# Kernel tuning notes

Hardware: AMD Instinct MI355X
Metric: run time of the kernel (lower is better)

## Reference

```python
import jax, jax.numpy as jnp
import numpy as np

N_NODES = 100000
N_EDGES = 1600000
NEG_SLOPE = 0.2  # PyG GATConv default
BN_EPS = 1e-5


def gat_conv(x, src, dst, W, a_src, a_dst, bias):
    # x: [N, F], W: [F, H, C]
    h = jnp.einsum('nf,fhc->nhc', x, W)                 # [N, H, C]
    al_src = jnp.sum(h * a_src, axis=-1)                # [N, H]
    al_dst = jnp.sum(h * a_dst, axis=-1)                # [N, H]
    e = al_src[src] + al_dst[dst]                       # [E, H]
    e = jnp.where(e >= 0, e, NEG_SLOPE * e)             # leaky_relu(0.2)
    # segment softmax over incoming edges of each dst node
    emax = jax.ops.segment_max(e, dst, num_segments=N_NODES)
    ee = jnp.exp(e - emax[dst])
    denom = jax.ops.segment_sum(ee, dst, num_segments=N_NODES)
    alpha = ee / denom[dst]                             # [E, H]
    msg = alpha[:, :, None] * h[src]                    # [E, H, C]
    out = jax.ops.segment_sum(msg, dst, num_segments=N_NODES)  # [N, H, C]
    return out.mean(axis=1) + bias                      # concat=False -> head mean


def batch_norm(x, gamma, beta):
    mu = jnp.mean(x, axis=0)
    var = jnp.var(x, axis=0)  # biased, as in torch BN normalization
    return (x - mu) * jax.lax.rsqrt(var + BN_EPS) * gamma + beta


def setup_inputs() -> dict:
    key = jax.random.key(0)
    ks = jax.random.split(key, 16)
    inp = {
        'x': jax.random.normal(ks[0], (N_NODES, 128), jnp.float32),
        'edge_index': jax.random.randint(ks[1], (2, N_EDGES), 0, N_NODES, jnp.int64)
            if jax.config.jax_enable_x64 else
            jax.random.randint(ks[1], (2, N_EDGES), 0, N_NODES, jnp.int32),
        'edge_attr': jax.random.normal(ks[2], (N_EDGES, 8), jnp.float32),
        'W0': 0.1 * jax.random.normal(ks[3], (128, 4, 32), jnp.float32),
        'a_src0': 0.1 * jax.random.normal(ks[4], (4, 32), jnp.float32),
        'a_dst0': 0.1 * jax.random.normal(ks[5], (4, 32), jnp.float32),
        'b0': jnp.zeros((32,), jnp.float32),
        'g0': jnp.ones((32,), jnp.float32),
        'be0': jnp.zeros((32,), jnp.float32),
        'W1': 0.1 * jax.random.normal(ks[6], (32, 4, 32), jnp.float32),
        'a_src1': 0.1 * jax.random.normal(ks[7], (4, 32), jnp.float32),
        'a_dst1': 0.1 * jax.random.normal(ks[8], (4, 32), jnp.float32),
        'b1': jnp.zeros((32,), jnp.float32),
        'g1': jnp.ones((32,), jnp.float32),
        'be1': jnp.zeros((32,), jnp.float32),
        'W2': 0.1 * jax.random.normal(ks[9], (32, 4, 32), jnp.float32),
        'a_src2': 0.1 * jax.random.normal(ks[10], (4, 32), jnp.float32),
        'a_dst2': 0.1 * jax.random.normal(ks[11], (4, 32), jnp.float32),
        'b2': jnp.zeros((32,), jnp.float32),
    }
    return inp


def reference(x, edge_index, edge_attr, W0, a_src0, a_dst0, b0, g0, be0,
              W1, a_src1, a_dst1, b1, g1, be1, W2, a_src2, a_dst2, b2):
    src, dst = edge_index[0], edge_index[1]
    h = gat_conv(x, src, dst, W0, a_src0, a_dst0, b0)
    h = jax.nn.relu(batch_norm(h, g0, be0))  # dropout = identity (deterministic ref)
    h = gat_conv(h, src, dst, W1, a_src1, a_dst1, b1)
    h = jax.nn.relu(batch_norm(h, g1, be1))
    h = gat_conv(h, src, dst, W2, a_src2, a_dst2, b2)
    return (h, edge_attr)
```

## Files before the change

kernel.cpp:

```cpp
#include <hip/hip_runtime.h>
#include <cstdio>
#include <cstdint>

#define LRELU 0.2f
#define BN_EPS 1e-5f

typedef short bf16x8 __attribute__((ext_vector_type(8)));
typedef float f32x4 __attribute__((ext_vector_type(4)));

__device__ inline unsigned short f2bf(float f) {
  unsigned int u = __float_as_uint(f);
  u += 0x7fffu + ((u >> 16) & 1u);
  return (unsigned short)(u >> 16);
}
__device__ inline float bf2f(unsigned short v) {
  return __uint_as_float(((unsigned int)v) << 16);
}
__device__ inline float bflo(unsigned int u) { return __uint_as_float(u << 16); }
__device__ inline float bfhi(unsigned int u) { return __uint_as_float(u & 0xffff0000u); }


__global__ __launch_bounds__(256) void k_bhist_copy(const int* __restrict__ dst,
                                                    int* __restrict__ bh,
                                                    const float4* __restrict__ ea,
                                                    float4* __restrict__ oea,
                                                    int E) {
  __shared__ int cnt[512];
  for (int b = threadIdx.x; b < 512; b += 256) cnt[b] = 0;
  __syncthreads();
  const int gid = blockIdx.x * blockDim.x + threadIdx.x;
  const int gstride = gridDim.x * blockDim.x;
  for (int i = gid; i < E; i += gstride) atomicAdd(&cnt[dst[i] >> 8], 1);
  const int n4 = E * 2;
  for (int i = gid; i < n4; i += gstride) oea[i] = ea[i];
  __syncthreads();
  for (int b = threadIdx.x; b < 512; b += 256)
    if (cnt[b]) atomicAdd(&bh[b], cnt[b]);
}

__global__ __launch_bounds__(512) void k_exscan(const int* __restrict__ bh,
                                                int* __restrict__ bstart,
                                                int* __restrict__ bcur, int n,
                                                int* __restrict__ offsN) {
  __shared__ int sh[512];
  const int t = threadIdx.x;
  int v = (t < n) ? bh[t] : 0;
  sh[t] = v;
  __syncthreads();
  for (int s = 1; s < 512; s <<= 1) {
    int u = (t >= s) ? sh[t - s] : 0;
    __syncthreads();
    sh[t] += u;
    __syncthreads();
  }
  if (t < n) {
    int ex = sh[t] - v;
    bstart[t] = ex;
    bcur[t] = ex;
  }
  if (t == n - 1) {
    bstart[n] = sh[t];
    *offsN = sh[t];
  }
}

__global__ __launch_bounds__(256) void k_bscatter(const int* __restrict__ src,
                                                  const int* __restrict__ dst,
                                                  int* __restrict__ bcur,
                                                  uint2* __restrict__ bpair, int E) {
  __shared__ int cnt[512];
  const int chunk = (E + gridDim.x - 1) / gridDim.x;
  const int beg = blockIdx.x * chunk;
  const int end = min(E, beg + chunk);
  for (int b = threadIdx.x; b < 512; b += 256) cnt[b] = 0;
  __syncthreads();
  for (int e = beg + threadIdx.x; e < end; e += 256)
    atomicAdd(&cnt[dst[e] >> 8], 1);
  __syncthreads();
  for (int b = threadIdx.x; b < 512; b += 256) {
    int c = cnt[b];
    cnt[b] = (c > 0) ? atomicAdd(&bcur[b], c) : 0;
  }
  __syncthreads();
  for (int e = beg + threadIdx.x; e < end; e += 256) {
    int d = dst[e];
    int pos = atomicAdd(&cnt[d >> 8], 1);
    bpair[pos] = make_uint2((unsigned)src[e], (unsigned)d);
  }
}

__global__ __launch_bounds__(256) void k_bcsr2(const uint2* __restrict__ bpair,
                                               const int* __restrict__ bstart,
                                               int* __restrict__ offs,
                                               int* __restrict__ srcs, int N) {
  __shared__ int sc[256];
  __shared__ int cur[256];
  const int b = blockIdx.x;
  const int lo = b << 8;
  const int t = threadIdx.x;
  const int e0 = bstart[b], e1 = bstart[b + 1];
  sc[t] = 0;
  __syncthreads();
  for (int e = e0 + t; e < e1; e += 256) atomicAdd(&sc[bpair[e].y & 255], 1);
  __syncthreads();
  int v = sc[t];
  for (int s = 1; s < 256; s <<= 1) {
    int u = (t >= s) ? sc[t - s] : 0;
    __syncthreads();
    sc[t] += u;
    __syncthreads();
  }
  const int pos0 = e0 + sc[t] - v;
  cur[t] = pos0;
  if (lo + t < N) offs[lo + t] = pos0;
  __syncthreads();
  for (int e = e0 + t; e < e1; e += 256) {
    uint2 p = bpair[e];
    int pos = atomicAdd(&cur[p.y & 255], 1);
    srcs[pos] = (int)p.x;
  }
}

__global__ void k_castW3(const float* __restrict__ W0, const float* __restrict__ W1,
                         const float* __restrict__ W2,
                         unsigned short* __restrict__ Wt0,
                         unsigned short* __restrict__ Wt1,
                         unsigned short* __restrict__ Wt2) {
  int o = blockIdx.x * 256 + threadIdx.x;
  if (o < 16384) {
    int n = o >> 7, k = o & 127;
    Wt0[o] = f2bf(W0[k * 128 + n]);
  } else if (o < 20480) {
    int p = o - 16384, n = p >> 5, k = p & 31;
    Wt1[p] = f2bf(W1[k * 128 + n]);
  } else if (o < 24576) {
    int p = o - 20480, n = p >> 5, k = p & 31;
    Wt2[p] = f2bf(W2[k * 128 + n]);
  }
}

template <int K, bool BN>
__global__ __launch_bounds__(256) void k_mfma(
    const float* __restrict__ Ain, const unsigned short* __restrict__ Wt,
    const float* __restrict__ asrc, const float* __restrict__ adst,
    const float* __restrict__ stats, const float* __restrict__ g,
    const float* __restrict__ be,
    unsigned short* __restrict__ h, float* __restrict__ als,
    float* __restrict__ ald, int N) {
  __shared__ unsigned short lsh[4][16 * 132];
  __shared__ float sc_s[32], sh_s[32];
  const int wv   = threadIdx.x >> 6;
  const int lane = threadIdx.x & 63;
  const int quad = lane >> 4;
  const int col  = lane & 15;
  const int m0   = blockIdx.x * 64 + wv * 16;
  const int rowc = min(m0 + col, N - 1);

  if constexpr (BN) {
    if (threadIdx.x < 32) {
      float s = 0.f, ss = 0.f;
#pragma unroll
      for (int r = 0; r < 8; r++) {
        s  += stats[r * 64 + threadIdx.x];
        ss += stats[r * 64 + 32 + threadIdx.x];
      }
      const float inv = 1.f / (float)N;
      const float mu = s * inv;
      const float var = ss * inv - mu * mu;
      const float scv = g[threadIdx.x] * rsqrtf(var + BN_EPS);
      sc_s[threadIdx.x] = scv;
      sh_s[threadIdx.x] = be[threadIdx.x] - mu * scv;
    }
    __syncthreads();
  }

  f32x4 acc[8];
#pragma unroll
  for (int t = 0; t < 8; t++) acc[t] = (f32x4){0.f, 0.f, 0.f, 0.f};

#pragma unroll
  for (int ks = 0; ks < K / 32; ks++) {
    const int k0 = ks * 32 + quad * 8;
    const float* ap = Ain + (size_t)rowc * K + k0;
    float4 f0 = *(const float4*)ap;
    float4 f1 = *(const float4*)(ap + 4);
    bf16x8 a;
    if constexpr (BN) {
      f0.x = fmaxf(0.f, fmaf(f0.x, sc_s[k0 + 0], sh_s[k0 + 0]));
      f0.y = fmaxf(0.f, fmaf(f0.y, sc_s[k0 + 1], sh_s[k0 + 1]));
      f0.z = fmaxf(0.f, fmaf(f0.z, sc_s[k0 + 2], sh_s[k0 + 2]));
      f0.w = fmaxf(0.f, fmaf(f0.w, sc_s[k0 + 3], sh_s[k0 + 3]));
      f1.x = fmaxf(0.f, fmaf(f1.x, sc_s[k0 + 4], sh_s[k0 + 4]));
      f1.y = fmaxf(0.f, fmaf(f1.y, sc_s[k0 + 5], sh_s[k0 + 5]));
      f1.z = fmaxf(0.f, fmaf(f1.z, sc_s[k0 + 6], sh_s[k0 + 6]));
      f1.w = fmaxf(0.f, fmaf(f1.w, sc_s[k0 + 7], sh_s[k0 + 7]));
    }
    a[0] = (short)f2bf(f0.x); a[1] = (short)f2bf(f0.y);
    a[2] = (short)f2bf(f0.z); a[3] = (short)f2bf(f0.w);
    a[4] = (short)f2bf(f1.x); a[5] = (short)f2bf(f1.y);
    a[6] = (short)f2bf(f1.z); a[7] = (short)f2bf(f1.w);
#pragma unroll
    for (int t = 0; t < 8; t++) {
      bf16x8 b = *(const bf16x8*)(Wt + (size_t)(t * 16 + col) * K + k0);
      acc[t] = __builtin_amdgcn_mfma_f32_16x16x32_bf16(a, b, acc[t], 0, 0, 0);
    }
  }

#pragma unroll
  for (int t = 0; t < 8; t++) {
#pragma unroll
    for (int j = 0; j < 4; j++)
      lsh[wv][(quad * 4 + j) * 132 + col + 16 * t] = f2bf(acc[t][j]);
  }
  __syncthreads();

  float as8[8], ad8[8];
#pragma unroll
  for (int j = 0; j < 8; j++) {
    as8[j] = asrc[col * 8 + j];
    ad8[j] = adst[col * 8 + j];
  }

#pragma unroll
  for (int i = 0; i < 4; i++) {
    const int row = i * 4 + quad;
    const int hrow = m0 + row;
    const unsigned short* rp = &lsh[wv][row * 132 + col * 8];
    ushort4 lo = *(const ushort4*)rp;
    ushort4 hi = *(const ushort4*)(rp + 4);
    float p = 0.f, q = 0.f, v;
    v = bf2f(lo.x); p += v * as8[0]; q += v * ad8[0];
    v = bf2f(lo.y); p += v * as8[1]; q += v * ad8[1];
    v = bf2f(lo.z); p += v * as8[2]; q += v * ad8[2];
    v = bf2f(lo.w); p += v * as8[3]; q += v * ad8[3];
    v = bf2f(hi.x); p += v * as8[4]; q += v * ad8[4];
    v = bf2f(hi.y); p += v * as8[5]; q += v * ad8[5];
    v = bf2f(hi.z); p += v * as8[6]; q += v * ad8[6];
    v = bf2f(hi.w); p += v * as8[7]; q += v * ad8[7];
    if (hrow < N) {
      ushort4* gp = (ushort4*)(h + (size_t)hrow * 128 + col * 8);
      gp[0] = lo; gp[1] = hi;
    }
    p += __shfl_xor(p, 1); p += __shfl_xor(p, 2);
    q += __shfl_xor(q, 1); q += __shfl_xor(q, 2);
    if ((lane & 3) == 0 && hrow < N) {
      const int head = col >> 2;
      als[hrow * 4 + head] = p;
      ald[hrow * 4 + head] = q;
    }
  }
}

template <bool STATS>
__global__ __launch_bounds__(256) void k_agg(
    const unsigned int* __restrict__ h2, const float* __restrict__ als,
    const float* __restrict__ ald, const int* __restrict__ offs,
    const int* __restrict__ srcs, const float* __restrict__ bias,
    float* __restrict__ y, float* __restrict__ stats, int N) {
  __shared__ float s1[32], s2[32];
  const int node = blockIdx.x * 4 + (threadIdx.x >> 6);
  const int lane = threadIdx.x & 63;
  const bool valid = node < N;
  if constexpr (STATS) {
    if (threadIdx.x < 32) { s1[threadIdx.x] = 0.f; s2[threadIdx.x] = 0.f; }
    __syncthreads();
  } else {
    if (!valid) return;
  }

  if (valid) {
    const int half = lane >> 5;
    const int sub  = lane & 31;
    const int head = sub >> 3;
    const int beg = __builtin_amdgcn_readfirstlane(offs[node]);
    const int end = __builtin_amdgcn_readfirstlane(offs[node + 1]);
    const float ad = ald[node * 4 + head];
    float ax0 = 0.f, ax1 = 0.f, ax2 = 0.f, ax3 = 0.f, dn = 0.f;

    for (int base = beg; base < end; base += 64) {
      const int mm = min(64, end - base);
      const int sv = srcs[base + min(lane, mm - 1)];
      const int vlim = mm - half;

      float aA0, aA1, aA2, aA3, aB0, aB1, aB2, aB3;
      uint2 uA0, uA1, uA2, uA3, uB0, uB1, uB2, uB3;
      int iA0, iA1, iA2, iA3, iB0, iB1, iB2, iB3;

#define SLOT(S, K, I)                                                      \
  {                                                                        \
    i##S##K = (I);                                                         \
    const int c0 = min((I), mm - 1), c1 = min((I) + 1, mm - 1);            \
    const int sA_ = __builtin_amdgcn_readlane(sv, c0);                     \
    const int sB_ = __builtin_amdgcn_readlane(sv, c1);                     \
    const int s_ = half ? sB_ : sA_;                                       \
    a##S##K = als[s_ * 4 + head];                                          \
    u##S##K = *(const uint2*)(h2 + (size_t)s_ * 64 + (sub << 1));          \
  }
#define ISSUE(S, J0) SLOT(S, 0, (J0)) SLOT(S, 1, (J0) + 2)                 \
                     SLOT(S, 2, (J0) + 4) SLOT(S, 3, (J0) + 6)
#define CSLOT(S, K)                                                        \
  {                                                                        \
    float e_ = a##S##K + ad;                                               \
    e_ = fmaxf(e_, LRELU * e_);                                            \
    float w_ = __expf(e_);                                                 \
    w_ = (i##S##K < vlim) ? w_ : 0.f;                                      \
    dn += w_;                                                              \
    ax0 = fmaf(w_, bflo(u##S##K.x), ax0);                                  \
    ax1 = fmaf(w_, bfhi(u##S##K.x), ax1);                                  \
    ax2 = fmaf(w_, bflo(u##S##K.y), ax2);                                  \
    ax3 = fmaf(w_, bfhi(u##S##K.y), ax3);                                  \
  }
#define COMPUTE(S) CSLOT(S, 0) CSLOT(S, 1) CSLOT(S, 2) CSLOT(S, 3)

      int j0 = 0;
      ISSUE(A, 0)
      j0 = 8;
      if (j0 >= mm) {
        COMPUTE(A)
      } else {
        for (;;) {
          ISSUE(B, j0) COMPUTE(A)
          j0 += 8;
          if (j0 >= mm) { COMPUTE(B) break; }
          ISSUE(A, j0) COMPUTE(B)
          j0 += 8;
          if (j0 >= mm) { COMPUTE(A) break; }
        }
      }
#undef SLOT
#undef ISSUE
#undef CSLOT
#undef COMPUTE
    }

    dn += __shfl_xor(dn, 32);
    const float r = (dn > 0.f) ? (1.f / dn) : 0.f;
    ax0 *= r; ax1 *= r; ax2 *= r; ax3 *= r;
    ax0 += __shfl_xor(ax0, 32); ax1 += __shfl_xor(ax1, 32);
    ax2 += __shfl_xor(ax2, 32); ax3 += __shfl_xor(ax3, 32);
    ax0 += __shfl_xor(ax0, 8);  ax1 += __shfl_xor(ax1, 8);
    ax2 += __shfl_xor(ax2, 8);  ax3 += __shfl_xor(ax3, 8);
    ax0 += __shfl_xor(ax0, 16); ax1 += __shfl_xor(ax1, 16);
    ax2 += __shfl_xor(ax2, 16); ax3 += __shfl_xor(ax3, 16);

    if (lane < 8) {
      float4 b4 = ((const float4*)bias)[lane];
      float4 o;
      o.x = 0.25f * ax0 + b4.x;
      o.y = 0.25f * ax1 + b4.y;
      o.z = 0.25f * ax2 + b4.z;
      o.w = 0.25f * ax3 + b4.w;
      ((float4*)(y + (size_t)node * 32))[lane] = o;
      if constexpr (STATS) {
        atomicAdd(&s1[4 * lane + 0], o.x); atomicAdd(&s2[4 * lane + 0], o.x * o.x);
        atomicAdd(&s1[4 * lane + 1], o.y); atomicAdd(&s2[4 * lane + 1], o.y * o.y);
        atomicAdd(&s1[4 * lane + 2], o.z); atomicAdd(&s2[4 * lane + 2], o.z * o.z);
        atomicAdd(&s1[4 * lane + 3], o.w); atomicAdd(&s2[4 * lane + 3], o.w * o.w);
      }
    }
  }

  if constexpr (STATS) {
    __syncthreads();
    if (threadIdx.x < 32) {
      float* sb = stats + (blockIdx.x & 7) * 64;
      atomicAdd(&sb[threadIdx.x], s1[threadIdx.x]);
      atomicAdd(&sb[32 + threadIdx.x], s2[threadIdx.x]);
    }
  }
}

extern "C" void kernel_launch(void* const* d_in, const int* in_sizes, int n_in,
                              void* d_out, int out_size, void* d_ws, size_t ws_size,
                              hipStream_t stream) {
  const float* x   = (const float*)d_in[0];
  const int*   ei  = (const int*)d_in[1];
  const float* ea  = (const float*)d_in[2];
  const float* W0  = (const float*)d_in[3];
  const float* as0 = (const float*)d_in[4];
  const float* ad0 = (const float*)d_in[5];
  const float* b0  = (const float*)d_in[6];
  const float* g0  = (const float*)d_in[7];
  const float* be0 = (const float*)d_in[8];
  const float* W1  = (const float*)d_in[9];
  const float* as1 = (const float*)d_in[10];
  const float* ad1 = (const float*)d_in[11];
  const float* b1  = (const float*)d_in[12];
  const float* g1  = (const float*)d_in[13];
  const float* be1 = (const float*)d_in[14];
  const float* W2  = (const float*)d_in[15];
  const float* as2 = (const float*)d_in[16];
  const float* ad2 = (const float*)d_in[17];
  const float* b2  = (const float*)d_in[18];

  const int N = in_sizes[0] / 128;
  const int E = in_sizes[1] / 2;
  const int* srcI = ei;
  const int* dstI = ei + E;
  const int NB = (N + 255) >> 8;

  char* w = (char*)d_ws;
  auto carve = [&](size_t bytes) -> void* {
    void* p = (void*)w;
    w += (bytes + 255) & ~(size_t)255;
    return p;
  };
  unsigned short* h  = (unsigned short*)carve((size_t)N * 128 * 2);
  float* als        = (float*)carve((size_t)N * 4 * 4);
  float* ald        = (float*)carve((size_t)N * 4 * 4);
  float* y          = (float*)carve((size_t)N * 32 * 4);
  int* offs         = (int*)carve((size_t)(N + 1) * 4);
  int* srcs         = (int*)carve((size_t)E * 4);
  int* bh           = (int*)carve(512 * 4);
  float* stats      = (float*)carve(1024 * 4);
  char* zend        = w;
  int* bstart       = (int*)carve(513 * 4);
  int* bcur         = (int*)carve(512 * 4);
  unsigned short* Wt0 = (unsigned short*)carve(128 * 128 * 2);
  unsigned short* Wt1 = (unsigned short*)carve(128 * 32 * 2);
  unsigned short* Wt2 = (unsigned short*)carve(128 * 32 * 2);
  if ((size_t)(w - (char*)d_ws) > ws_size) {
    fprintf(stderr, "GAT kernel: ws too small (%zu needed, %zu given)\n",
            (size_t)(w - (char*)d_ws), ws_size);
    return;
  }
  uint2* bpair = (uint2*)h;

  float* out_nodes = (float*)d_out;
  float* out_ea    = out_nodes + (size_t)N * 32;

  hipMemsetAsync(bh, 0, (size_t)(zend - (char*)bh), stream);

  k_bhist_copy<<<256, 256, 0, stream>>>(dstI, bh, (const float4*)ea,
                                        (float4*)out_ea, E);
  k_exscan<<<1, 512, 0, stream>>>(bh, bstart, bcur, NB, offs + N);
  k_bscatter<<<128, 256, 0, stream>>>(srcI, dstI, bcur, bpair, E);
  k_bcsr2<<<NB, 256, 0, stream>>>(bpair, bstart, offs, srcs, N);

  k_castW3<<<96, 256, 0, stream>>>(W0, W1, W2, Wt0, Wt1, Wt2);

  const int gGemm = (N + 63) / 64;
  const int gAgg  = (N + 3) / 4;

  k_mfma<128, false><<<gGemm, 256, 0, stream>>>(x, Wt0, as0, ad0,
                                                nullptr, nullptr, nullptr,
                                                h, als, ald, N);
  k_agg<true><<<gAgg, 256, 0, stream>>>((const unsigned int*)h, als, ald, offs,
                                        srcs, b0, y, stats, N);
  k_mfma<32, true><<<gGemm, 256, 0, stream>>>(y, Wt1, as1, ad1, stats, g0, be0,
                                              h, als, ald, N);
  k_agg<true><<<gAgg, 256, 0, stream>>>((const unsigned int*)h, als, ald, offs,
                                        srcs, b1, y, stats + 512, N);
  k_mfma<32, true><<<gGemm, 256, 0, stream>>>(y, Wt2, as2, ad2, stats + 512, g1, be1,
                                              h, als, ald, N);
  k_agg<false><<<gAgg, 256, 0, stream>>>((const unsigned int*)h, als, ald, offs,
                                         srcs, b2, out_nodes, nullptr, N);
}
```

Measured before the change: 612.4 us.

## Fuse CSR build and weight cast into one persistent kernel with grid barriers

Merges the histogram/copy, exclusive scan, bucket scatter, per-bucket CSR, and weight-cast kernels into a single kernel launched with NB (391) blocks. Phases are separated by software grid barriers on atomic counters. Each block redundantly recomputes the 512-entry bucket scan in shared memory, and the dst histogram is recomputed per chunk. The aim is to remove several launch gaps and small serial kernels. The cost is that correctness depends on all blocks being co-resident; with 391 blocks of 256 threads on MI355X this should hold, but it is not guaranteed.

```diff
diff --git a/kernel.cpp b/kernel.cpp
--- a/kernel.cpp
+++ b/kernel.cpp
@@ -19,93 +19,111 @@
 __device__ inline float bflo(unsigned int u) { return __uint_as_float(u << 16); }
 __device__ inline float bfhi(unsigned int u) { return __uint_as_float(u & 0xffff0000u); }
 
-
-__global__ __launch_bounds__(256) void k_bhist_copy(const int* __restrict__ dst,
-                                                    int* __restrict__ bh,
-                                                    const float4* __restrict__ ea,
-                                                    float4* __restrict__ oea,
-                                                    int E) {
+__device__ inline void gbar(int* ctr, int target) {
+  __syncthreads();
+  if (threadIdx.x == 0) {
+    __threadfence();
+    __hip_atomic_fetch_add(ctr, 1, __ATOMIC_ACQ_REL, __HIP_MEMORY_SCOPE_AGENT);
+    while (__hip_atomic_load(ctr, __ATOMIC_ACQUIRE,
+                             __HIP_MEMORY_SCOPE_AGENT) < target)
+      __builtin_amdgcn_s_sleep(16);
+  }
+  __syncthreads();
+}
+
+__global__ __launch_bounds__(256) void k_build(
+    const int* __restrict__ src, const int* __restrict__ dst,
+    const float4* __restrict__ ea, float4* __restrict__ oea,
+    const float* __restrict__ W0, const float* __restrict__ W1,
+    const float* __restrict__ W2,
+    unsigned short* __restrict__ Wt0, unsigned short* __restrict__ Wt1,
+    unsigned short* __restrict__ Wt2,
+    int* __restrict__ bh, int* __restrict__ bclaim,
+    uint2* __restrict__ bpair,
+    int* __restrict__ offs, int* __restrict__ srcs,
+    int* __restrict__ sync, int E, int N, int NB) {
   __shared__ int cnt[512];
-  for (int b = threadIdx.x; b < 512; b += 256) cnt[b] = 0;
-  __syncthreads();
-  const int gid = blockIdx.x * blockDim.x + threadIdx.x;
-  const int gstride = gridDim.x * blockDim.x;
-  for (int i = gid; i < E; i += gstride) atomicAdd(&cnt[dst[i] >> 8], 1);
-  const int n4 = E * 2;
-  for (int i = gid; i < n4; i += gstride) oea[i] = ea[i];
-  __syncthreads();
-  for (int b = threadIdx.x; b < 512; b += 256)
-    if (cnt[b]) atomicAdd(&bh[b], cnt[b]);
-}
-
-__global__ __launch_bounds__(512) void k_exscan(const int* __restrict__ bh,
-                                                int* __restrict__ bstart,
-                                                int* __restrict__ bcur, int n,
-                                                int* __restrict__ offsN) {
-  __shared__ int sh[512];
+  __shared__ int pre[256];
+  __shared__ int bsc[513];
+  __shared__ int sc[256];
+  __shared__ int cur[256];
   const int t = threadIdx.x;
-  int v = (t < n) ? bh[t] : 0;
-  sh[t] = v;
-  __syncthreads();
-  for (int s = 1; s < 512; s <<= 1) {
-    int u = (t >= s) ? sh[t - s] : 0;
-    __syncthreads();
-    sh[t] += u;
-    __syncthreads();
-  }
-  if (t < n) {
-    int ex = sh[t] - v;
-    bstart[t] = ex;
-    bcur[t] = ex;
-  }
-  if (t == n - 1) {
-    bstart[n] = sh[t];
-    *offsN = sh[t];
-  }
-}
-
-__global__ __launch_bounds__(256) void k_bscatter(const int* __restrict__ src,
-                                                  const int* __restrict__ dst,
-                                                  int* __restrict__ bcur,
-                                                  uint2* __restrict__ bpair, int E) {
-  __shared__ int cnt[512];
-  const int chunk = (E + gridDim.x - 1) / gridDim.x;
+  const int G = gridDim.x;
+  const int gid = blockIdx.x * 256 + t;
+
+  if (gid < 24576) {
+    int o = gid;
+    if (o < 16384) {
+      int n = o >> 7, k = o & 127;
+      Wt0[o] = f2bf(W0[k * 128 + n]);
+    } else if (o < 20480) {
+      int p = o - 16384, n = p >> 5, k = p & 31;
+      Wt1[p] = f2bf(W1[k * 128 + n]);
+    } else {
+      int p = o - 20480, n = p >> 5, k = p & 31;
+      Wt2[p] = f2bf(W2[k * 128 + n]);
+    }
+  }
+
+  const int chunk = (E + G - 1) / G;
   const int beg = blockIdx.x * chunk;
   const int end = min(E, beg + chunk);
-  for (int b = threadIdx.x; b < 512; b += 256) cnt[b] = 0;
-  __syncthreads();
-  for (int e = beg + threadIdx.x; e < end; e += 256)
-    atomicAdd(&cnt[dst[e] >> 8], 1);
-  __syncthreads();
-  for (int b = threadIdx.x; b < 512; b += 256) {
+  for (int b = t; b < 512; b += 256) cnt[b] = 0;
+  __syncthreads();
+  for (int e = beg + t; e < end; e += 256) atomicAdd(&cnt[dst[e] >> 8], 1);
+  const int n4 = E * 2;
+  for (int i = gid; i < n4; i += G * 256) oea[i] = ea[i];
+  __syncthreads();
+  for (int b = t; b < 512; b += 256)
+    if (cnt[b]) atomicAdd(&bh[b], cnt[b]);
+
+  gbar(&sync[0], G);
+
+  const int a0 = bh[2 * t];
+  const int a1 = bh[2 * t + 1];
+  int s = a0 + a1;
+  pre[t] = s;
+  __syncthreads();
+  for (int st = 1; st < 256; st <<= 1) {
+    int u = (t >= st) ? pre[t - st] : 0;
+    __syncthreads();
+    pre[t] += u;
+    __syncthreads();
+  }
+  const int ex = pre[t] - s;
+  bsc[2 * t] = ex;
+  bsc[2 * t + 1] = ex + a0;
+  if (t == 255) bsc[512] = pre[255];
+  __syncthreads();
+
+  for (int b = t; b < 512; b += 256) cnt[b] = 0;
+  __syncthreads();
+  for (int e = beg + t; e < end; e += 256) atomicAdd(&cnt[dst[e] >> 8], 1);
+  __syncthreads();
+  for (int b = t; b < 512; b += 256) {
     int c = cnt[b];
-    cnt[b] = (c > 0) ? atomicAdd(&bcur[b], c) : 0;
-  }
-  __syncthreads();
-  for (int e = beg + threadIdx.x; e < end; e += 256) {
+    cnt[b] = (c > 0) ? (bsc[b] + atomicAdd(&bclaim[b], c)) : 0;
+  }
+  __syncthreads();
+  for (int e = beg + t; e < end; e += 256) {
     int d = dst[e];
     int pos = atomicAdd(&cnt[d >> 8], 1);
     bpair[pos] = make_uint2((unsigned)src[e], (unsigned)d);
   }
-}
-
-__global__ __launch_bounds__(256) void k_bcsr2(const uint2* __restrict__ bpair,
-                                               const int* __restrict__ bstart,
-                                               int* __restrict__ offs,
-                                               int* __restrict__ srcs, int N) {
-  __shared__ int sc[256];
-  __shared__ int cur[256];
+
+  gbar(&sync[1], G);
+
   const int b = blockIdx.x;
+  if (b >= NB) return;
   const int lo = b << 8;
-  const int t = threadIdx.x;
-  const int e0 = bstart[b], e1 = bstart[b + 1];
+  const int e0 = bsc[b], e1 = bsc[b + 1];
   sc[t] = 0;
   __syncthreads();
   for (int e = e0 + t; e < e1; e += 256) atomicAdd(&sc[bpair[e].y & 255], 1);
   __syncthreads();
   int v = sc[t];
-  for (int s = 1; s < 256; s <<= 1) {
-    int u = (t >= s) ? sc[t - s] : 0;
+  for (int st = 1; st < 256; st <<= 1) {
+    int u = (t >= st) ? sc[t - st] : 0;
     __syncthreads();
     sc[t] += u;
     __syncthreads();
@@ -113,29 +131,12 @@
   const int pos0 = e0 + sc[t] - v;
   cur[t] = pos0;
   if (lo + t < N) offs[lo + t] = pos0;
+  if (b == 0 && t == 0) offs[N] = E;
   __syncthreads();
   for (int e = e0 + t; e < e1; e += 256) {
     uint2 p = bpair[e];
     int pos = atomicAdd(&cur[p.y & 255], 1);
     srcs[pos] = (int)p.x;
-  }
-}
-
-__global__ void k_castW3(const float* __restrict__ W0, const float* __restrict__ W1,
-                         const float* __restrict__ W2,
-                         unsigned short* __restrict__ Wt0,
-                         unsigned short* __restrict__ Wt1,
-                         unsigned short* __restrict__ Wt2) {
-  int o = blockIdx.x * 256 + threadIdx.x;
-  if (o < 16384) {
-    int n = o >> 7, k = o & 127;
-    Wt0[o] = f2bf(W0[k * 128 + n]);
-  } else if (o < 20480) {
-    int p = o - 16384, n = p >> 5, k = p & 31;
-    Wt1[p] = f2bf(W1[k * 128 + n]);
-  } else if (o < 24576) {
-    int p = o - 20480, n = p >> 5, k = p & 31;
-    Wt2[p] = f2bf(W2[k * 128 + n]);
   }
 }
 
@@ -412,10 +413,10 @@
   int* offs         = (int*)carve((size_t)(N + 1) * 4);
   int* srcs         = (int*)carve((size_t)E * 4);
   int* bh           = (int*)carve(512 * 4);
+  int* bclaim       = (int*)carve(512 * 4);
   float* stats      = (float*)carve(1024 * 4);
+  int* syncc        = (int*)carve(16 * 4);
   char* zend        = w;
-  int* bstart       = (int*)carve(513 * 4);
-  int* bcur         = (int*)carve(512 * 4);
   unsigned short* Wt0 = (unsigned short*)carve(128 * 128 * 2);
   unsigned short* Wt1 = (unsigned short*)carve(128 * 32 * 2);
   unsigned short* Wt2 = (unsigned short*)carve(128 * 32 * 2);
@@ -429,15 +430,12 @@
   float* out_nodes = (float*)d_out;
   float* out_ea    = out_nodes + (size_t)N * 32;
 
-  hipMemsetAsync(bh, 0, (size_t)(zend - (char*)bh), stream);
-
-  k_bhist_copy<<<256, 256, 0, stream>>>(dstI, bh, (const float4*)ea,
-                                        (float4*)out_ea, E);
-  k_exscan<<<1, 512, 0, stream>>>(bh, bstart, bcur, NB, offs + N);
-  k_bscatter<<<128, 256, 0, stream>>>(srcI, dstI, bcur, bpair, E);
-  k_bcsr2<<<NB, 256, 0, stream>>>(bpair, bstart, offs, srcs, N);
-
-  k_castW3<<<96, 256, 0, stream>>>(W0, W1, W2, Wt0, Wt1, Wt2);
+  (void)hipMemsetAsync(bh, 0, (size_t)(zend - (char*)bh), stream);
+
+  k_build<<<NB, 256, 0, stream>>>(srcI, dstI, (const float4*)ea,
+                                  (float4*)out_ea, W0, W1, W2, Wt0, Wt1, Wt2,
+                                  bh, bclaim, bpair, offs, srcs, syncc,
+                                  E, N, NB);
 
   const int gGemm = (N + 63) / 64;
   const int gAgg  = (N + 3) / 4;
```

After: 709.3 us. 1.16x slower.
